# Kernel optimization log

Hardware: AMD Instinct MI355X
Metric: run time of the kernel (lower is better)

## Reference

```python
import jax, jax.numpy as jnp
import numpy as np

N = 10000           # nodes
E = 160000          # edges
MUL = 128           # multiplicity of each irrep (128x0e + 128x1o)
EDGE_FEAT = 8       # radial embedding dim
AVG_NUM_NEIGHBORS = 16.0
MLP_IN = MUL + MUL + EDGE_FEAT + 1  # 265
NUM_W = 4 * MUL     # irreps_mid num_irreps = 256x0e + 256x1o -> 512 path weights
SQ3 = float(np.sqrt(3.0))


def setup_inputs() -> dict:
    key = jax.random.key(0)
    ks = jax.random.split(key, 16)
    node_feats = jax.random.normal(ks[0], (N, 4 * MUL), dtype=jnp.float32)  # [N,512] = 128x0e ++ 128x1o
    edge_attrs = jax.random.normal(ks[1], (E, 4), dtype=jnp.float32)        # 1x0e ++ 1x1o
    edge_feats = jax.random.normal(ks[2], (E, EDGE_FEAT), dtype=jnp.float32)
    lengths = jax.random.uniform(ks[3], (E, 1), dtype=jnp.float32)
    edge_index = jax.random.randint(ks[4], (2, E), 0, N, dtype=jnp.int32)
    # e3nn Linear weights (stored unit-variance; forward applies 1/sqrt(fan_in))
    W_scalar = jax.random.normal(ks[5], (MUL, MUL), dtype=jnp.float32)
    W_up0 = jax.random.normal(ks[6], (MUL, MUL), dtype=jnp.float32)
    W_up1 = jax.random.normal(ks[7], (MUL, MUL), dtype=jnp.float32)
    # conv_tp_weights MLP (flax Dense: fan-scaled init, bias on first two layers)
    W1 = jax.random.normal(ks[8], (MLP_IN, MUL), dtype=jnp.float32) / np.sqrt(MLP_IN)
    b1 = jnp.zeros((MUL,), dtype=jnp.float32)
    W2 = jax.random.normal(ks[9], (MUL, MUL), dtype=jnp.float32) / np.sqrt(MUL)
    b2 = jnp.zeros((MUL,), dtype=jnp.float32)
    W3 = jax.random.normal(ks[10], (MUL, NUM_W), dtype=jnp.float32) / np.sqrt(MUL)
    # final e3nn Linear: 256x0e+256x1o -> 128x0e+128x1o
    Wout0 = jax.random.normal(ks[11], (2 * MUL, MUL), dtype=jnp.float32)
    Wout1 = jax.random.normal(ks[12], (2 * MUL, MUL), dtype=jnp.float32)
    return {"node_feats": node_feats, "edge_attrs": edge_attrs, "edge_feats": edge_feats,
            "lengths": lengths, "edge_index": edge_index, "W_scalar": W_scalar,
            "W_up0": W_up0, "W_up1": W_up1, "W1": W1, "b1": b1, "W2": W2, "b2": b2,
            "W3": W3, "Wout0": Wout0, "Wout1": Wout1}


def reference(node_feats, edge_attrs, edge_feats, lengths, edge_index,
              W_scalar, W_up0, W_up1, W1, b1, W2, b2, W3, Wout0, Wout1):
    n = node_feats.shape[0]
    inv = 1.0 / np.sqrt(MUL)
    x0 = node_feats[:, :MUL]                       # [N,128]   0e
    x1 = node_feats[:, MUL:].reshape(n, MUL, 3)    # [N,128,3] 1o

    # linear_scalar: only 0e->0e path survives
    scalars = (x0 @ W_scalar) * inv                # [N,128]
    # linear_up: per-irrep channel mixing
    h0 = (x0 @ W_up0) * inv                        # [N,128]
    h1 = jnp.einsum('nmi,mo->noi', x1, W_up1) * inv  # [N,128,3]

    sender, receiver = edge_index[0], edge_index[1]

    # conv_tp_weights MLP
    mlp_in = jnp.concatenate([scalars[sender], scalars[receiver], edge_feats, lengths], axis=-1)
    h = jax.nn.silu(mlp_in @ W1 + b1)
    h = jax.nn.silu(h @ W2 + b2)
    tpw = h @ W3                                   # [E,512]

    xs0 = h0[sender]                               # [E,128]
    xs1 = h1[sender]                               # [E,128,3]
    y0 = edge_attrs[:, 0:1]                        # [E,1]  0e
    y1 = edge_attrs[:, 1:4]                        # [E,3]  1o

    # CG tensor product (component normalization), filtered to {0e,1o}; sorted order:
    # 0e block = [0e*0e->0e, 1o*1o->0e], 1o block = [0e*1o->1o, 1o*0e->1o]
    mA = xs0 * y0                                       # [E,128]   0e
    mD = (xs1 * y1[:, None, :]).sum(-1) / SQ3           # [E,128]   0e
    mB = xs0[:, :, None] * y1[:, None, :]               # [E,128,3] 1o
    mC = xs1 * y0[:, :, None]                           # [E,128,3] 1o

    # per-irrep path weights (one scalar per irrep channel)
    wA, wD = tpw[:, :MUL], tpw[:, MUL:2 * MUL]
    wB, wC = tpw[:, 2 * MUL:3 * MUL], tpw[:, 3 * MUL:]

    m0 = jnp.concatenate([mA * wA, mD * wD], axis=1)                          # [E,256]
    m1 = jnp.concatenate([mB * wB[:, :, None], mC * wC[:, :, None]], axis=1)  # [E,256,3]

    # scatter-sum aggregation to receivers
    agg0 = jax.ops.segment_sum(m0, receiver, num_segments=n)  # [N,256]
    agg1 = jax.ops.segment_sum(m1, receiver, num_segments=n)  # [N,256,3]

    # final e3nn Linear + / avg_num_neighbors
    scale = 1.0 / (np.sqrt(2 * MUL) * AVG_NUM_NEIGHBORS)
    out0 = (agg0 @ Wout0) * scale                             # [N,128]
    out1 = jnp.einsum('nmi,mo->noi', agg1, Wout1) * scale     # [N,128,3]

    # reshape_irreps: [N, mul, sum(ir dims)] = [N,128,4]
    return jnp.concatenate([out0[:, :, None], out1], axis=-1)
```

## Files before the change

kernel.cpp:

```cpp
#include <hip/hip_runtime.h>
#include <hip/hip_bf16.h>

#define NN 10000
#define NE 160000
#define TILE 32
#define A1S 296
#define A2S 136

typedef __attribute__((ext_vector_type(8))) short short8;
typedef __attribute__((ext_vector_type(4))) float f32x4;

__device__ __forceinline__ float silu_f(float x) { return x / (1.0f + __expf(-x)); }
__device__ __forceinline__ unsigned short bf16u(float v) {
    __hip_bfloat16 b = __float2bfloat16(v);
    return *reinterpret_cast<unsigned short*>(&b);
}
__device__ __forceinline__ short8 pack8(float4 a, float4 b) {
    short8 r;
    r[0]=(short)bf16u(a.x); r[1]=(short)bf16u(a.y); r[2]=(short)bf16u(a.z); r[3]=(short)bf16u(a.w);
    r[4]=(short)bf16u(b.x); r[5]=(short)bf16u(b.y); r[6]=(short)bf16u(b.z); r[7]=(short)bf16u(b.w);
    return r;
}
__device__ __forceinline__ void lds_barrier() {
    asm volatile("s_waitcnt lgkmcnt(0)" ::: "memory");
    __builtin_amdgcn_s_barrier();
    asm volatile("" ::: "memory");
}

#define OFF_W1  0
#define OFF_W2  36864
#define OFF_W3  53248
#define OFF_WSC 118784
#define OFF_WU0 135168
#define OFF_WU1 151552
#define OFF_WO0 167936
#define OFF_WO1 200704
#define WP_TOTAL 233472

__global__ __launch_bounds__(256) void convert_weights(
    const float* __restrict__ W1, const float* __restrict__ W2,
    const float* __restrict__ W3, const float* __restrict__ Wsc,
    const float* __restrict__ Wu0, const float* __restrict__ Wu1,
    const float* __restrict__ Wo0, const float* __restrict__ Wo1,
    unsigned short* __restrict__ wp,
    const int* __restrict__ edge_index, int* __restrict__ deg)
{
    int idx = blockIdx.x * 256 + threadIdx.x;
    if (idx < NE) atomicAdd(&deg[edge_index[NE + idx]], 1);
    if (idx >= WP_TOTAL) return;
    const float* src; int off, N, K;
    if      (idx < OFF_W2)  { src = W1;  off = OFF_W1;  N = 128; K = 265; }
    else if (idx < OFF_W3)  { src = W2;  off = OFF_W2;  N = 128; K = 128; }
    else if (idx < OFF_WSC) { src = W3;  off = OFF_W3;  N = 512; K = 128; }
    else if (idx < OFF_WU0) { src = Wsc; off = OFF_WSC; N = 128; K = 128; }
    else if (idx < OFF_WU1) { src = Wu0; off = OFF_WU0; N = 128; K = 128; }
    else if (idx < OFF_WO0) { src = Wu1; off = OFF_WU1; N = 128; K = 128; }
    else if (idx < OFF_WO1) { src = Wo0; off = OFF_WO0; N = 128; K = 256; }
    else                    { src = Wo1; off = OFF_WO1; N = 128; K = 256; }
    int j = idx - off;
    int kt = j / (N * 32);
    int rem = j % (N * 32);
    int n = rem >> 5, kk = rem & 31;
    int k = kt * 32 + kk;
    wp[idx] = (k < K) ? bf16u(src[k * N + n]) : (unsigned short)0;
}

__global__ __launch_bounds__(256) void node_transform(
    const float* __restrict__ node_feats,
    const unsigned short* __restrict__ wp,
    unsigned short* __restrict__ scalars_bf,
    unsigned short* __restrict__ hall)
{
    __shared__ unsigned short xls[4 * 16 * 136];
    const int t = threadIdx.x;
    const int bn = blockIdx.x * 16;

    for (int i = t; i < 16 * 512; i += 256) {
        int n = i >> 9, j = i & 511;
        unsigned short u = bf16u(node_feats[(size_t)(bn + n) * 512 + j]);
        if (j < 128) xls[n * 136 + j] = u;
        else {
            int jj = j - 128;
            int m = jj / 3;
            int c = jj - 3 * m;
            xls[(1 + c) * 2176 + n * 136 + m] = u;
        }
    }
    __syncthreads();

    const int wv = t >> 6, lane = t & 63, l16 = lane & 15, l4 = lane >> 4;
    const unsigned short* Wscp = wp + OFF_WSC;
    const unsigned short* Wu0p = wp + OFF_WU0;
    const unsigned short* Wu1p = wp + OFF_WU1;

    f32x4 asc[2] = {}, ah0[2] = {}, ah1[3][2] = {};
    for (int kt = 0; kt < 4; ++kt) {
        short8 ax0 = *(const short8*)(xls + l16 * 136 + kt * 32 + l4 * 8);
        short8 ax1[3];
        #pragma unroll
        for (int c = 0; c < 3; ++c)
            ax1[c] = *(const short8*)(xls + (1 + c) * 2176 + l16 * 136 + kt * 32 + l4 * 8);
        #pragma unroll
        for (int n = 0; n < 2; ++n) {
            int col = wv * 32 + n * 16 + l16;
            short8 bsc = *(const short8*)(Wscp + ((size_t)kt * 128 + col) * 32 + l4 * 8);
            short8 bu0 = *(const short8*)(Wu0p + ((size_t)kt * 128 + col) * 32 + l4 * 8);
            short8 bu1 = *(const short8*)(Wu1p + ((size_t)kt * 128 + col) * 32 + l4 * 8);
            asc[n] = __builtin_amdgcn_mfma_f32_16x16x32_bf16(ax0, bsc, asc[n], 0, 0, 0);
            ah0[n] = __builtin_amdgcn_mfma_f32_16x16x32_bf16(ax0, bu0, ah0[n], 0, 0, 0);
            #pragma unroll
            for (int c = 0; c < 3; ++c)
                ah1[c][n] = __builtin_amdgcn_mfma_f32_16x16x32_bf16(ax1[c], bu1, ah1[c][n], 0, 0, 0);
        }
    }
    const float inv = 0.08838834764831845f;
    #pragma unroll
    for (int n = 0; n < 2; ++n) {
        int col = wv * 32 + n * 16 + l16;
        #pragma unroll
        for (int r = 0; r < 4; ++r) {
            int node = bn + l4 * 4 + r;
            scalars_bf[(size_t)node * 128 + col] = bf16u(asc[n][r] * inv);
            unsigned int lo = (unsigned int)bf16u(ah0[n][r] * inv)
                            | ((unsigned int)bf16u(ah1[0][n][r] * inv) << 16);
            unsigned int hi = (unsigned int)bf16u(ah1[1][n][r] * inv)
                            | ((unsigned int)bf16u(ah1[2][n][r] * inv) << 16);
            *(uint2*)(hall + ((size_t)node * 128 + col) * 4) = make_uint2(lo, hi);
        }
    }
}

__global__ __launch_bounds__(1024) void scan_kernel(const int* __restrict__ deg,
                                                    int* __restrict__ cursor) {
    __shared__ int s[1024];
    const int t = threadIdx.x;
    const int base = t * 10;
    int ld[10];
    int lsum = 0;
    #pragma unroll
    for (int i = 0; i < 10; ++i) {
        int idx = base + i;
        ld[i] = (idx < NN) ? deg[idx] : 0;
        lsum += ld[i];
    }
    s[t] = lsum;
    __syncthreads();
    for (int off = 1; off < 1024; off <<= 1) {
        int u = (t >= off) ? s[t - off] : 0;
        __syncthreads();
        s[t] += u;
        __syncthreads();
    }
    int run = s[t] - lsum;
    #pragma unroll
    for (int i = 0; i < 10; ++i) {
        int idx = base + i;
        if (idx < NN) cursor[idx] = run;
        run += ld[i];
    }
}

__global__ __launch_bounds__(256) void perm_kernel(const int* __restrict__ edge_index,
                                                   int* __restrict__ cursor,
                                                   int* __restrict__ perm) {
    int e = blockIdx.x * 256 + threadIdx.x;
    if (e < NE) {
        int r = edge_index[NE + e];
        int pos = atomicAdd(&cursor[r], 1);
        perm[pos] = e;
    }
}

__global__ __launch_bounds__(256, 5) void edge_kernel(
    const unsigned short* __restrict__ scalars_bf,
    const unsigned short* __restrict__ hall,
    const float* __restrict__ edge_attrs,
    const float* __restrict__ edge_feats,
    const float* __restrict__ lengths,
    const int* __restrict__ edge_index,
    const int* __restrict__ perm,
    const float* __restrict__ b1, const float* __restrict__ b2,
    const unsigned short* __restrict__ wp,
    float* __restrict__ agg0, float* __restrict__ agg1t)
{
    __shared__ unsigned char smem_u[27648];
    __shared__ int   eid_s[TILE];
    __shared__ int   s_s[TILE];
    __shared__ int   r_s[TILE];
    __shared__ float4 y_s[TILE];

    unsigned short* A1 = (unsigned short*)smem_u;
    unsigned short* A2 = (unsigned short*)(smem_u + 18944);
    unsigned short* A3 = A1;
    float* PKh = (float*)(smem_u + 8704);

    const int t = threadIdx.x;
    const int e0 = blockIdx.x * TILE;
    const int wv = t >> 6;
    const int lane = t & 63;
    const int l16 = lane & 15;
    const int l4 = lane >> 4;

    if (t < TILE) {
        int eid = perm[e0 + t];
        eid_s[t] = eid;
        s_s[t] = edge_index[eid];
        r_s[t] = edge_index[NE + eid];
        y_s[t] = *(const float4*)(edge_attrs + (size_t)eid * 4);
    }
    __syncthreads();

    {
        const int e = t >> 3, j = t & 7;
        const unsigned short* srow = scalars_bf + (size_t)s_s[e] * 128;
        const unsigned short* rrow = scalars_bf + (size_t)r_s[e] * 128;
        *(uint4*)(A1 + e*A1S + j*16)       = *(const uint4*)(srow + j*16);
        *(uint4*)(A1 + e*A1S + j*16 + 8)   = *(const uint4*)(srow + j*16 + 8);
        *(uint4*)(A1 + e*A1S + 128 + j*16)     = *(const uint4*)(rrow + j*16);
        *(uint4*)(A1 + e*A1S + 128 + j*16 + 8) = *(const uint4*)(rrow + j*16 + 8);
        A1[e*A1S + 256 + j] = bf16u(edge_feats[(size_t)eid_s[e] * 8 + j]);
        if (t < TILE) A1[t*A1S + 264] = bf16u(lengths[eid_s[t]]);
        for (int i = t; i < TILE * 23; i += 256) {
            int row = i / 23, c = 265 + (i - row * 23);
            A1[row*A1S + c] = 0;
        }
    }

    const int q = t >> 6, o = t & 63;
    const int rlo = q * 8;
    uint2 pfA[8], pfB[8];
    #pragma unroll
    for (int i = 0; i < 8; ++i)
        pfA[i] = *(const uint2*)(hall + ((size_t)s_s[rlo + i] * 128 + o) * 4);
    __syncthreads();

    const unsigned short* Wp1 = wp + OFF_W1;
    const unsigned short* Wp2 = wp + OFF_W2;
    const unsigned short* Wp3 = wp + OFF_W3;

    {
        f32x4 acc[2][2] = {};
        for (int kt = 0; kt < 9; ++kt) {
            short8 a0 = *(const short8*)(A1 + (     l16)*A1S + kt*32 + l4*8);
            short8 a1 = *(const short8*)(A1 + (16 + l16)*A1S + kt*32 + l4*8);
            #pragma unroll
            for (int n = 0; n < 2; ++n) {
                int col = (2*wv + n)*16 + l16;
                short8 b = *(const short8*)(Wp1 + ((size_t)kt*128 + col)*32 + l4*8);
                acc[0][n] = __builtin_amdgcn_mfma_f32_16x16x32_bf16(a0, b, acc[0][n], 0, 0, 0);
                acc[1][n] = __builtin_amdgcn_mfma_f32_16x16x32_bf16(a1, b, acc[1][n], 0, 0, 0);
            }
        }
        #pragma unroll
        for (int n = 0; n < 2; ++n) {
            int col = (2*wv + n)*16 + l16;
            float bb = b1[col];
            #pragma unroll
            for (int m = 0; m < 2; ++m)
                #pragma unroll
                for (int r = 0; r < 4; ++r) {
                    int row = m*16 + l4*4 + r;
                    A2[row*A2S + col] = bf16u(silu_f(acc[m][n][r] + bb));
                }
        }
    }
    __syncthreads();

    {
        f32x4 acc[2][2] = {};
        for (int kt = 0; kt < 4; ++kt) {
            short8 a0 = *(const short8*)(A2 + (     l16)*A2S + kt*32 + l4*8);
            short8 a1 = *(const short8*)(A2 + (16 + l16)*A2S + kt*32 + l4*8);
            #pragma unroll
            for (int n = 0; n < 2; ++n) {
                int col = (2*wv + n)*16 + l16;
                short8 b = *(const short8*)(Wp2 + ((size_t)kt*128 + col)*32 + l4*8);
                acc[0][n] = __builtin_amdgcn_mfma_f32_16x16x32_bf16(a0, b, acc[0][n], 0, 0, 0);
                acc[1][n] = __builtin_amdgcn_mfma_f32_16x16x32_bf16(a1, b, acc[1][n], 0, 0, 0);
            }
        }
        #pragma unroll
        for (int n = 0; n < 2; ++n) {
            int col = (2*wv + n)*16 + l16;
            float bb = b2[col];
            #pragma unroll
            for (int m = 0; m < 2; ++m)
                #pragma unroll
                for (int r = 0; r < 4; ++r) {
                    int row = m*16 + l4*4 + r;
                    A3[row*A2S + col] = bf16u(silu_f(acc[m][n][r] + bb));
                }
        }
    }
    __syncthreads();

    const float rs3 = 0.57735026918962576f;
    auto do_seg = [&](const int pass, const int hh, const uint2* pf) {
        const int base0 = pass ? 128 : 0;
        const int base1 = pass ? 384 : 256;
        f32x4 acc[2][2] = {};
        for (int kt = 0; kt < 4; ++kt) {
            short8 a0 = *(const short8*)(A3 + (     l16)*A2S + kt*32 + l4*8);
            short8 a1 = *(const short8*)(A3 + (16 + l16)*A2S + kt*32 + l4*8);
            #pragma unroll
            for (int fam = 0; fam < 2; ++fam) {
                int col = (fam ? base1 : base0) + hh*64 + wv*16 + l16;
                short8 b = *(const short8*)(Wp3 + ((size_t)kt*512 + col)*32 + l4*8);
                acc[fam][0] = __builtin_amdgcn_mfma_f32_16x16x32_bf16(a0, b, acc[fam][0], 0, 0, 0);
                acc[fam][1] = __builtin_amdgcn_mfma_f32_16x16x32_bf16(a1, b, acc[fam][1], 0, 0, 0);
            }
        }
        #pragma unroll
        for (int fam = 0; fam < 2; ++fam)
            #pragma unroll
            for (int m = 0; m < 2; ++m)
                #pragma unroll
                for (int r = 0; r < 4; ++r) {
                    int row = m*16 + l4*4 + r;
                    float y0 = y_s[row].x;
                    float fold = (fam == 0) ? (pass ? rs3 : y0) : (pass ? y0 : 1.0f);
                    PKh[row*132 + fam*64 + wv*16 + l16] = acc[fam][m][r] * fold;
                }
        lds_barrier();

        {
            const int ocol = hh*64 + o;
            float ac0 = 0.f, ac1 = 0.f, ac2 = 0.f, ac3 = 0.f;
            int run_start = rlo;
            int prev_rn = r_s[rlo];

            auto flush = [&](int rn, bool interior) {
                size_t b0 = (size_t)rn * 256 + base0 + ocol;
                if (interior) {
                    agg0[b0] = ac0;
                    agg1t[0*(size_t)NN*256 + b0] = ac1;
                    agg1t[1*(size_t)NN*256 + b0] = ac2;
                    agg1t[2*(size_t)NN*256 + b0] = ac3;
                } else {
                    atomicAdd(agg0 + b0, ac0);
                    atomicAdd(agg1t + 0*(size_t)NN*256 + b0, ac1);
                    atomicAdd(agg1t + 1*(size_t)NN*256 + b0, ac2);
                    atomicAdd(agg1t + 2*(size_t)NN*256 + b0, ac3);
                }
            };

            #pragma unroll
            for (int i = 0; i < 8; ++i) {
                int row = rlo + i;
                int rn = r_s[row];
                if (rn != prev_rn) {
                    flush(prev_rn, run_start > rlo);
                    ac0 = ac1 = ac2 = ac3 = 0.f;
                    run_start = row;
                    prev_rn = rn;
                }
                float w0 = PKh[row*132 + o];
                float w1 = PKh[row*132 + 64 + o];
                float4 y = y_s[row];
                if (pass == 0) {
                    float x = __uint_as_float(pf[i].x << 16);
                    ac0 = fmaf(x, w0, ac0);
                    float xb = x * w1;
                    ac1 = fmaf(xb, y.y, ac1);
                    ac2 = fmaf(xb, y.z, ac2);
                    ac3 = fmaf(xb, y.w, ac3);
                } else {
                    float xx = __uint_as_float(pf[i].x & 0xffff0000u);
                    float xy = __uint_as_float(pf[i].y << 16);
                    float xz = __uint_as_float(pf[i].y & 0xffff0000u);
                    float dd = xx*y.y + xy*y.z + xz*y.w;
                    ac0 = fmaf(dd, w0, ac0);
                    ac1 = fmaf(xx, w1, ac1);
                    ac2 = fmaf(xy, w1, ac2);
                    ac3 = fmaf(xz, w1, ac3);
                }
            }
            flush(prev_rn, false);
        }
        lds_barrier();
    };

    do_seg(0, 0, pfA);
    do_seg(1, 0, pfA);
    #pragma unroll
    for (int i = 0; i < 8; ++i)
        pfB[i] = *(const uint2*)(hall + ((size_t)s_s[rlo + i] * 128 + 64 + o) * 4);
    do_seg(0, 1, pfB);
    do_seg(1, 1, pfB);
}

__global__ __launch_bounds__(256) void output_transform(
    const float* __restrict__ agg0,
    const float* __restrict__ agg1t,
    const unsigned short* __restrict__ wp,
    float* __restrict__ out)
{
    __shared__ unsigned short As[4][16 * 264];
    const int t = threadIdx.x;
    const int bn = blockIdx.x * 16;

    for (int i = t; i < 2048; i += 256) {
        int mat = i >> 9;
        int rem = i & 511;
        int n = rem >> 5;
        int ko = (rem & 31) * 8;
        const float* src = (mat == 0)
            ? (agg0 + (size_t)(bn + n) * 256 + ko)
            : (agg1t + (size_t)(mat - 1) * NN * 256 + (size_t)(bn + n) * 256 + ko);
        float4 v0 = *(const float4*)(src);
        float4 v1 = *(const float4*)(src + 4);
        *(short8*)(&As[mat][n * 264 + ko]) = pack8(v0, v1);
    }
    __syncthreads();

    const int wv = t >> 6, lane = t & 63, l16 = lane & 15, l4 = lane >> 4;
    const unsigned short* Wo0p = wp + OFF_WO0;
    const unsigned short* Wo1p = wp + OFF_WO1;

    f32x4 acc[2][4] = {};
    for (int kt = 0; kt < 8; ++kt) {
        short8 a0 = *(const short8*)(&As[0][l16 * 264 + kt * 32 + l4 * 8]);
        short8 a1 = *(const short8*)(&As[1][l16 * 264 + kt * 32 + l4 * 8]);
        short8 a2 = *(const short8*)(&As[2][l16 * 264 + kt * 32 + l4 * 8]);
        short8 a3 = *(const short8*)(&As[3][l16 * 264 + kt * 32 + l4 * 8]);
        #pragma unroll
        for (int n = 0; n < 2; ++n) {
            int col = wv * 32 + n * 16 + l16;
            short8 bw0 = *(const short8*)(Wo0p + ((size_t)kt * 128 + col) * 32 + l4 * 8);
            short8 bw1 = *(const short8*)(Wo1p + ((size_t)kt * 128 + col) * 32 + l4 * 8);
            acc[n][0] = __builtin_amdgcn_mfma_f32_16x16x32_bf16(a0, bw0, acc[n][0], 0, 0, 0);
            acc[n][1] = __builtin_amdgcn_mfma_f32_16x16x32_bf16(a1, bw1, acc[n][1], 0, 0, 0);
            acc[n][2] = __builtin_amdgcn_mfma_f32_16x16x32_bf16(a2, bw1, acc[n][2], 0, 0, 0);
            acc[n][3] = __builtin_amdgcn_mfma_f32_16x16x32_bf16(a3, bw1, acc[n][3], 0, 0, 0);
        }
    }
    const float scale = 0.00390625f;
    #pragma unroll
    for (int n = 0; n < 2; ++n) {
        int col = wv * 32 + n * 16 + l16;
        #pragma unroll
        for (int r = 0; r < 4; ++r) {
            int node = bn + l4 * 4 + r;
            float4 v = make_float4(acc[n][0][r] * scale, acc[n][1][r] * scale,
                                   acc[n][2][r] * scale, acc[n][3][r] * scale);
            *(float4*)(out + ((size_t)node * 128 + col) * 4) = v;
        }
    }
}

extern "C" void kernel_launch(void* const* d_in, const int* in_sizes, int n_in,
                              void* d_out, int out_size, void* d_ws, size_t ws_size,
                              hipStream_t stream) {
    const float* node_feats = (const float*)d_in[0];
    const float* edge_attrs = (const float*)d_in[1];
    const float* edge_feats = (const float*)d_in[2];
    const float* lengths    = (const float*)d_in[3];
    const int*   edge_index = (const int*)d_in[4];
    const float* W_scalar   = (const float*)d_in[5];
    const float* W_up0      = (const float*)d_in[6];
    const float* W_up1      = (const float*)d_in[7];
    const float* W1         = (const float*)d_in[8];
    const float* b1         = (const float*)d_in[9];
    const float* W2         = (const float*)d_in[10];
    const float* b2         = (const float*)d_in[11];
    const float* W3         = (const float*)d_in[12];
    const float* Wout0      = (const float*)d_in[13];
    const float* Wout1      = (const float*)d_in[14];

    float* ws = (float*)d_ws;
    unsigned short* scalars_bf = (unsigned short*)ws;
    unsigned short* hall = (unsigned short*)(ws + 640000);
    float* agg0  = ws + 3200000;
    float* agg1t = ws + 5760000;
    int* deg    = (int*)(ws + 13440000);
    int* cursor = (int*)(ws + 13450000);
    int* perm   = (int*)(ws + 13460000);
    unsigned short* wpack = (unsigned short*)(ws + 13620000);
    if (ws_size < 13736736ull * 4ull) return;

    hipMemsetAsync(agg0, 0, 10250000ull * 4ull, stream);
    convert_weights<<<(WP_TOTAL + 255) / 256, 256, 0, stream>>>(
        W1, W2, W3, W_scalar, W_up0, W_up1, Wout0, Wout1, wpack, edge_index, deg);
    node_transform<<<625, 256, 0, stream>>>(node_feats, wpack, scalars_bf, hall);
    scan_kernel<<<1, 1024, 0, stream>>>(deg, cursor);
    perm_kernel<<<(NE + 255) / 256, 256, 0, stream>>>(edge_index, cursor, perm);
    edge_kernel<<<NE / TILE, 256, 0, stream>>>(scalars_bf, hall, edge_attrs, edge_feats, lengths,
                                               edge_index, perm, b1, b2, wpack, agg0, agg1t);
    output_transform<<<625, 256, 0, stream>>>(agg0, agg1t, wpack, (float*)d_out);
}
```

Measured before the change: 207.6 us.

## Process multiple edge tiles per block with prefetch, fold agg zeroing into node kernel

The edge kernel becomes persistent over four tiles per block. Each tile's indices and gathered scalar rows are double-buffered and prefetched while the previous tile's MLP runs, so gather latency is hidden behind the matrix work. The large memset of the aggregation buffers is replaced by zeroing inside node_transform, and only the degree array is memset. The trade-off is four times fewer edge blocks, which may reduce load balance and occupancy, plus extra register pressure from the prefetched values.

```diff
diff --git a/kernel.cpp b/kernel.cpp
--- a/kernel.cpp
+++ b/kernel.cpp
@@ -4,6 +4,7 @@
 #define NN 10000
 #define NE 160000
 #define TILE 32
+#define TPB 4
 #define A1S 296
 #define A2S 136
 
@@ -69,11 +70,25 @@
     const float* __restrict__ node_feats,
     const unsigned short* __restrict__ wp,
     unsigned short* __restrict__ scalars_bf,
-    unsigned short* __restrict__ hall)
+    unsigned short* __restrict__ hall,
+    float* __restrict__ agg0, float* __restrict__ agg1t)
 {
     __shared__ unsigned short xls[4 * 16 * 136];
     const int t = threadIdx.x;
     const int bn = blockIdx.x * 16;
+
+    {
+        const float4 z = make_float4(0.f, 0.f, 0.f, 0.f);
+        float4* a0 = (float4*)(agg0 + (size_t)bn * 256);
+        #pragma unroll
+        for (int i = 0; i < 4; ++i) a0[t + 256 * i] = z;
+        #pragma unroll
+        for (int c = 0; c < 3; ++c) {
+            float4* a1 = (float4*)(agg1t + (size_t)c * NN * 256 + (size_t)bn * 256);
+            #pragma unroll
+            for (int i = 0; i < 4; ++i) a1[t + 256 * i] = z;
+        }
+    }
 
     for (int i = t; i < 16 * 512; i += 256) {
         int n = i >> 9, j = i & 511;
@@ -184,10 +199,10 @@
     float* __restrict__ agg0, float* __restrict__ agg1t)
 {
     __shared__ unsigned char smem_u[27648];
-    __shared__ int   eid_s[TILE];
-    __shared__ int   s_s[TILE];
-    __shared__ int   r_s[TILE];
-    __shared__ float4 y_s[TILE];
+    __shared__ int   eid_s[2][TILE];
+    __shared__ int   s_s[2][TILE];
+    __shared__ int   r_s[2][TILE];
+    __shared__ float4 y_s[2][TILE];
 
     unsigned short* A1 = (unsigned short*)smem_u;
     unsigned short* A2 = (unsigned short*)(smem_u + 18944);
@@ -195,198 +210,235 @@
     float* PKh = (float*)(smem_u + 8704);
 
     const int t = threadIdx.x;
-    const int e0 = blockIdx.x * TILE;
     const int wv = t >> 6;
     const int lane = t & 63;
     const int l16 = lane & 15;
     const int l4 = lane >> 4;
+    const int q = t >> 6, o = t & 63;
+    const int rlo = q * 8;
+    const int es = t >> 3, j8 = t & 7;
+
+    const int tile0 = blockIdx.x * TPB;
+
+    const unsigned short* Wp1 = wp + OFF_W1;
+    const unsigned short* Wp2 = wp + OFF_W2;
+    const unsigned short* Wp3 = wp + OFF_W3;
+    const float rs3 = 0.57735026918962576f;
+
+    int h_eid = 0, h_s = 0, h_r = 0; float4 h_y = make_float4(0,0,0,0);
+    uint4 sv0, sv1, rv0, rv1; float efreg; float lenreg;
 
     if (t < TILE) {
-        int eid = perm[e0 + t];
-        eid_s[t] = eid;
-        s_s[t] = edge_index[eid];
-        r_s[t] = edge_index[NE + eid];
-        y_s[t] = *(const float4*)(edge_attrs + (size_t)eid * 4);
-    }
-    __syncthreads();
-
+        int eid = perm[tile0 * TILE + t];
+        eid_s[0][t] = eid;
+        s_s[0][t] = edge_index[eid];
+        r_s[0][t] = edge_index[NE + eid];
+        y_s[0][t] = *(const float4*)(edge_attrs + (size_t)eid * 4);
+    }
+    lds_barrier();
     {
-        const int e = t >> 3, j = t & 7;
-        const unsigned short* srow = scalars_bf + (size_t)s_s[e] * 128;
-        const unsigned short* rrow = scalars_bf + (size_t)r_s[e] * 128;
-        *(uint4*)(A1 + e*A1S + j*16)       = *(const uint4*)(srow + j*16);
-        *(uint4*)(A1 + e*A1S + j*16 + 8)   = *(const uint4*)(srow + j*16 + 8);
-        *(uint4*)(A1 + e*A1S + 128 + j*16)     = *(const uint4*)(rrow + j*16);
-        *(uint4*)(A1 + e*A1S + 128 + j*16 + 8) = *(const uint4*)(rrow + j*16 + 8);
-        A1[e*A1S + 256 + j] = bf16u(edge_feats[(size_t)eid_s[e] * 8 + j]);
-        if (t < TILE) A1[t*A1S + 264] = bf16u(lengths[eid_s[t]]);
+        const unsigned short* srow = scalars_bf + (size_t)s_s[0][es] * 128;
+        const unsigned short* rrow = scalars_bf + (size_t)r_s[0][es] * 128;
+        sv0 = *(const uint4*)(srow + j8*16);
+        sv1 = *(const uint4*)(srow + j8*16 + 8);
+        rv0 = *(const uint4*)(rrow + j8*16);
+        rv1 = *(const uint4*)(rrow + j8*16 + 8);
+        efreg = edge_feats[(size_t)eid_s[0][es] * 8 + j8];
+        lenreg = (t < TILE) ? lengths[eid_s[0][t]] : 0.f;
+    }
+
+    #pragma unroll 1
+    for (int j = 0; j < TPB; ++j) {
+        const int cur = j & 1, nxt = cur ^ 1;
+
+        *(uint4*)(A1 + es*A1S + j8*16)       = sv0;
+        *(uint4*)(A1 + es*A1S + j8*16 + 8)   = sv1;
+        *(uint4*)(A1 + es*A1S + 128 + j8*16)     = rv0;
+        *(uint4*)(A1 + es*A1S + 128 + j8*16 + 8) = rv1;
+        A1[es*A1S + 256 + j8] = bf16u(efreg);
+        if (t < TILE) A1[t*A1S + 264] = bf16u(lenreg);
         for (int i = t; i < TILE * 23; i += 256) {
             int row = i / 23, c = 265 + (i - row * 23);
             A1[row*A1S + c] = 0;
         }
-    }
-
-    const int q = t >> 6, o = t & 63;
-    const int rlo = q * 8;
-    uint2 pfA[8], pfB[8];
-    #pragma unroll
-    for (int i = 0; i < 8; ++i)
-        pfA[i] = *(const uint2*)(hall + ((size_t)s_s[rlo + i] * 128 + o) * 4);
-    __syncthreads();
-
-    const unsigned short* Wp1 = wp + OFF_W1;
-    const unsigned short* Wp2 = wp + OFF_W2;
-    const unsigned short* Wp3 = wp + OFF_W3;
-
-    {
-        f32x4 acc[2][2] = {};
-        for (int kt = 0; kt < 9; ++kt) {
-            short8 a0 = *(const short8*)(A1 + (     l16)*A1S + kt*32 + l4*8);
-            short8 a1 = *(const short8*)(A1 + (16 + l16)*A1S + kt*32 + l4*8);
+
+        uint2 pfA[8], pfB[8];
+        #pragma unroll
+        for (int i = 0; i < 8; ++i)
+            pfA[i] = *(const uint2*)(hall + ((size_t)s_s[cur][rlo + i] * 128 + o) * 4);
+
+        if (j + 1 < TPB && t < TILE) {
+            h_eid = perm[(tile0 + j + 1) * TILE + t];
+            h_s = edge_index[h_eid];
+            h_r = edge_index[NE + h_eid];
+            h_y = *(const float4*)(edge_attrs + (size_t)h_eid * 4);
+        }
+
+        lds_barrier();
+
+        {
+            f32x4 acc[2][2] = {};
+            for (int kt = 0; kt < 9; ++kt) {
+                short8 a0 = *(const short8*)(A1 + (     l16)*A1S + kt*32 + l4*8);
+                short8 a1 = *(const short8*)(A1 + (16 + l16)*A1S + kt*32 + l4*8);
+                #pragma unroll
+                for (int n = 0; n < 2; ++n) {
+                    int col = (2*wv + n)*16 + l16;
+                    short8 b = *(const short8*)(Wp1 + ((size_t)kt*128 + col)*32 + l4*8);
+                    acc[0][n] = __builtin_amdgcn_mfma_f32_16x16x32_bf16(a0, b, acc[0][n], 0, 0, 0);
+                    acc[1][n] = __builtin_amdgcn_mfma_f32_16x16x32_bf16(a1, b, acc[1][n], 0, 0, 0);
+                }
+            }
             #pragma unroll
             for (int n = 0; n < 2; ++n) {
                 int col = (2*wv + n)*16 + l16;
-                short8 b = *(const short8*)(Wp1 + ((size_t)kt*128 + col)*32 + l4*8);
-                acc[0][n] = __builtin_amdgcn_mfma_f32_16x16x32_bf16(a0, b, acc[0][n], 0, 0, 0);
-                acc[1][n] = __builtin_amdgcn_mfma_f32_16x16x32_bf16(a1, b, acc[1][n], 0, 0, 0);
+                float bb = b1[col];
+                #pragma unroll
+                for (int m = 0; m < 2; ++m)
+                    #pragma unroll
+                    for (int r = 0; r < 4; ++r) {
+                        int row = m*16 + l4*4 + r;
+                        A2[row*A2S + col] = bf16u(silu_f(acc[m][n][r] + bb));
+                    }
             }
         }
-        #pragma unroll
-        for (int n = 0; n < 2; ++n) {
-            int col = (2*wv + n)*16 + l16;
-            float bb = b1[col];
-            #pragma unroll
-            for (int m = 0; m < 2; ++m)
-                #pragma unroll
-                for (int r = 0; r < 4; ++r) {
-                    int row = m*16 + l4*4 + r;
-                    A2[row*A2S + col] = bf16u(silu_f(acc[m][n][r] + bb));
+        if (j + 1 < TPB && t < TILE) {
+            eid_s[nxt][t] = h_eid; s_s[nxt][t] = h_s; r_s[nxt][t] = h_r; y_s[nxt][t] = h_y;
+        }
+        lds_barrier();
+
+        if (j + 1 < TPB) {
+            const unsigned short* srow = scalars_bf + (size_t)s_s[nxt][es] * 128;
+            const unsigned short* rrow = scalars_bf + (size_t)r_s[nxt][es] * 128;
+            sv0 = *(const uint4*)(srow + j8*16);
+            sv1 = *(const uint4*)(srow + j8*16 + 8);
+            rv0 = *(const uint4*)(rrow + j8*16);
+            rv1 = *(const uint4*)(rrow + j8*16 + 8);
+            efreg = edge_feats[(size_t)eid_s[nxt][es] * 8 + j8];
+            lenreg = (t < TILE) ? lengths[eid_s[nxt][t]] : 0.f;
+        }
+
+        {
+            f32x4 acc[2][2] = {};
+            for (int kt = 0; kt < 4; ++kt) {
+                short8 a0 = *(const short8*)(A2 + (     l16)*A2S + kt*32 + l4*8);
+                short8 a1 = *(const short8*)(A2 + (16 + l16)*A2S + kt*32 + l4*8);
+                #pragma unroll
+                for (int n = 0; n < 2; ++n) {
+                    int col = (2*wv + n)*16 + l16;
+                    short8 b = *(const short8*)(Wp2 + ((size_t)kt*128 + col)*32 + l4*8);
+                    acc[0][n] = __builtin_amdgcn_mfma_f32_16x16x32_bf16(a0, b, acc[0][n], 0, 0, 0);
+                    acc[1][n] = __builtin_amdgcn_mfma_f32_16x16x32_bf16(a1, b, acc[1][n], 0, 0, 0);
                 }
-        }
-    }
-    __syncthreads();
-
-    {
-        f32x4 acc[2][2] = {};
-        for (int kt = 0; kt < 4; ++kt) {
-            short8 a0 = *(const short8*)(A2 + (     l16)*A2S + kt*32 + l4*8);
-            short8 a1 = *(const short8*)(A2 + (16 + l16)*A2S + kt*32 + l4*8);
+            }
             #pragma unroll
             for (int n = 0; n < 2; ++n) {
                 int col = (2*wv + n)*16 + l16;
-                short8 b = *(const short8*)(Wp2 + ((size_t)kt*128 + col)*32 + l4*8);
-                acc[0][n] = __builtin_amdgcn_mfma_f32_16x16x32_bf16(a0, b, acc[0][n], 0, 0, 0);
-                acc[1][n] = __builtin_amdgcn_mfma_f32_16x16x32_bf16(a1, b, acc[1][n], 0, 0, 0);
+                float bb = b2[col];
+                #pragma unroll
+                for (int m = 0; m < 2; ++m)
+                    #pragma unroll
+                    for (int r = 0; r < 4; ++r) {
+                        int row = m*16 + l4*4 + r;
+                        A3[row*A2S + col] = bf16u(silu_f(acc[m][n][r] + bb));
+                    }
             }
         }
-        #pragma unroll
-        for (int n = 0; n < 2; ++n) {
-            int col = (2*wv + n)*16 + l16;
-            float bb = b2[col];
-            #pragma unroll
-            for (int m = 0; m < 2; ++m)
-                #pragma unroll
-                for (int r = 0; r < 4; ++r) {
-                    int row = m*16 + l4*4 + r;
-                    A3[row*A2S + col] = bf16u(silu_f(acc[m][n][r] + bb));
-                }
-        }
-    }
-    __syncthreads();
-
-    const float rs3 = 0.57735026918962576f;
-    auto do_seg = [&](const int pass, const int hh, const uint2* pf) {
-        const int base0 = pass ? 128 : 0;
-        const int base1 = pass ? 384 : 256;
-        f32x4 acc[2][2] = {};
-        for (int kt = 0; kt < 4; ++kt) {
-            short8 a0 = *(const short8*)(A3 + (     l16)*A2S + kt*32 + l4*8);
-            short8 a1 = *(const short8*)(A3 + (16 + l16)*A2S + kt*32 + l4*8);
-            #pragma unroll
-            for (int fam = 0; fam < 2; ++fam) {
-                int col = (fam ? base1 : base0) + hh*64 + wv*16 + l16;
-                short8 b = *(const short8*)(Wp3 + ((size_t)kt*512 + col)*32 + l4*8);
-                acc[fam][0] = __builtin_amdgcn_mfma_f32_16x16x32_bf16(a0, b, acc[fam][0], 0, 0, 0);
-                acc[fam][1] = __builtin_amdgcn_mfma_f32_16x16x32_bf16(a1, b, acc[fam][1], 0, 0, 0);
-            }
-        }
-        #pragma unroll
-        for (int fam = 0; fam < 2; ++fam)
-            #pragma unroll
-            for (int m = 0; m < 2; ++m)
-                #pragma unroll
-                for (int r = 0; r < 4; ++r) {
-                    int row = m*16 + l4*4 + r;
-                    float y0 = y_s[row].x;
-                    float fold = (fam == 0) ? (pass ? rs3 : y0) : (pass ? y0 : 1.0f);
-                    PKh[row*132 + fam*64 + wv*16 + l16] = acc[fam][m][r] * fold;
-                }
         lds_barrier();
 
-        {
-            const int ocol = hh*64 + o;
-            float ac0 = 0.f, ac1 = 0.f, ac2 = 0.f, ac3 = 0.f;
-            int run_start = rlo;
-            int prev_rn = r_s[rlo];
-
-            auto flush = [&](int rn, bool interior) {
-                size_t b0 = (size_t)rn * 256 + base0 + ocol;
-                if (interior) {
-                    agg0[b0] = ac0;
-                    agg1t[0*(size_t)NN*256 + b0] = ac1;
-                    agg1t[1*(size_t)NN*256 + b0] = ac2;
-                    agg1t[2*(size_t)NN*256 + b0] = ac3;
-                } else {
-                    atomicAdd(agg0 + b0, ac0);
-                    atomicAdd(agg1t + 0*(size_t)NN*256 + b0, ac1);
-                    atomicAdd(agg1t + 1*(size_t)NN*256 + b0, ac2);
-                    atomicAdd(agg1t + 2*(size_t)NN*256 + b0, ac3);
-                }
-            };
-
-            #pragma unroll
-            for (int i = 0; i < 8; ++i) {
-                int row = rlo + i;
-                int rn = r_s[row];
-                if (rn != prev_rn) {
-                    flush(prev_rn, run_start > rlo);
-                    ac0 = ac1 = ac2 = ac3 = 0.f;
-                    run_start = row;
-                    prev_rn = rn;
-                }
-                float w0 = PKh[row*132 + o];
-                float w1 = PKh[row*132 + 64 + o];
-                float4 y = y_s[row];
-                if (pass == 0) {
-                    float x = __uint_as_float(pf[i].x << 16);
-                    ac0 = fmaf(x, w0, ac0);
-                    float xb = x * w1;
-                    ac1 = fmaf(xb, y.y, ac1);
-                    ac2 = fmaf(xb, y.z, ac2);
-                    ac3 = fmaf(xb, y.w, ac3);
-                } else {
-                    float xx = __uint_as_float(pf[i].x & 0xffff0000u);
-                    float xy = __uint_as_float(pf[i].y << 16);
-                    float xz = __uint_as_float(pf[i].y & 0xffff0000u);
-                    float dd = xx*y.y + xy*y.z + xz*y.w;
-                    ac0 = fmaf(dd, w0, ac0);
-                    ac1 = fmaf(xx, w1, ac1);
-                    ac2 = fmaf(xy, w1, ac2);
-                    ac3 = fmaf(xz, w1, ac3);
+        auto do_seg = [&](const int pass, const int hh, const uint2* pf) {
+            const int base0 = pass ? 128 : 0;
+            const int base1 = pass ? 384 : 256;
+            f32x4 acc[2][2] = {};
+            for (int kt = 0; kt < 4; ++kt) {
+                short8 a0 = *(const short8*)(A3 + (     l16)*A2S + kt*32 + l4*8);
+                short8 a1 = *(const short8*)(A3 + (16 + l16)*A2S + kt*32 + l4*8);
+                #pragma unroll
+                for (int fam = 0; fam < 2; ++fam) {
+                    int col = (fam ? base1 : base0) + hh*64 + wv*16 + l16;
+                    short8 b = *(const short8*)(Wp3 + ((size_t)kt*512 + col)*32 + l4*8);
+                    acc[fam][0] = __builtin_amdgcn_mfma_f32_16x16x32_bf16(a0, b, acc[fam][0], 0, 0, 0);
+                    acc[fam][1] = __builtin_amdgcn_mfma_f32_16x16x32_bf16(a1, b, acc[fam][1], 0, 0, 0);
                 }
             }
-            flush(prev_rn, false);
-        }
-        lds_barrier();
-    };
-
-    do_seg(0, 0, pfA);
-    do_seg(1, 0, pfA);
-    #pragma unroll
-    for (int i = 0; i < 8; ++i)
-        pfB[i] = *(const uint2*)(hall + ((size_t)s_s[rlo + i] * 128 + 64 + o) * 4);
-    do_seg(0, 1, pfB);
-    do_seg(1, 1, pfB);
+            #pragma unroll
+            for (int fam = 0; fam < 2; ++fam)
+                #pragma unroll
+                for (int m = 0; m < 2; ++m)
+                    #pragma unroll
+                    for (int r = 0; r < 4; ++r) {
+                        int row = m*16 + l4*4 + r;
+                        float y0 = y_s[cur][row].x;
+                        float fold = (fam == 0) ? (pass ? rs3 : y0) : (pass ? y0 : 1.0f);
+                        PKh[row*132 + fam*64 + wv*16 + l16] = acc[fam][m][r] * fold;
+                    }
+            lds_barrier();
+
+            {
+                const int ocol = hh*64 + o;
+                float ac0 = 0.f, ac1 = 0.f, ac2 = 0.f, ac3 = 0.f;
+                int run_start = rlo;
+                int prev_rn = r_s[cur][rlo];
+
+                auto flush = [&](int rn, bool interior) {
+                    size_t b0 = (size_t)rn * 256 + base0 + ocol;
+                    if (interior) {
+                        agg0[b0] = ac0;
+                        agg1t[0*(size_t)NN*256 + b0] = ac1;
+                        agg1t[1*(size_t)NN*256 + b0] = ac2;
+                        agg1t[2*(size_t)NN*256 + b0] = ac3;
+                    } else {
+                        atomicAdd(agg0 + b0, ac0);
+                        atomicAdd(agg1t + 0*(size_t)NN*256 + b0, ac1);
+                        atomicAdd(agg1t + 1*(size_t)NN*256 + b0, ac2);
+                        atomicAdd(agg1t + 2*(size_t)NN*256 + b0, ac3);
+                    }
+                };
+
+                #pragma unroll
+                for (int i = 0; i < 8; ++i) {
+                    int row = rlo + i;
+                    int rn = r_s[cur][row];
+                    if (rn != prev_rn) {
+                        flush(prev_rn, run_start > rlo);
+                        ac0 = ac1 = ac2 = ac3 = 0.f;
+                        run_start = row;
+                        prev_rn = rn;
+                    }
+                    float w0 = PKh[row*132 + o];
+                    float w1 = PKh[row*132 + 64 + o];
+                    float4 y = y_s[cur][row];
+                    if (pass == 0) {
+                        float x = __uint_as_float(pf[i].x << 16);
+                        ac0 = fmaf(x, w0, ac0);
+                        float xb = x * w1;
+                        ac1 = fmaf(xb, y.y, ac1);
+                        ac2 = fmaf(xb, y.z, ac2);
+                        ac3 = fmaf(xb, y.w, ac3);
+                    } else {
+                        float xx = __uint_as_float(pf[i].x & 0xffff0000u);
+                        float xy = __uint_as_float(pf[i].y << 16);
+                        float xz = __uint_as_float(pf[i].y & 0xffff0000u);
+                        float dd = xx*y.y + xy*y.z + xz*y.w;
+                        ac0 = fmaf(dd, w0, ac0);
+                        ac1 = fmaf(xx, w1, ac1);
+                        ac2 = fmaf(xy, w1, ac2);
+                        ac3 = fmaf(xz, w1, ac3);
+                    }
+                }
+                flush(prev_rn, false);
+            }
+            lds_barrier();
+        };
+
+        do_seg(0, 0, pfA);
+        do_seg(1, 0, pfA);
+        #pragma unroll
+        for (int i = 0; i < 8; ++i)
+            pfB[i] = *(const uint2*)(hall + ((size_t)s_s[cur][rlo + i] * 128 + 64 + o) * 4);
+        do_seg(0, 1, pfB);
+        do_seg(1, 1, pfB);
+    }
 }
 
 __global__ __launch_bounds__(256) void output_transform(
@@ -478,13 +530,13 @@
     unsigned short* wpack = (unsigned short*)(ws + 13620000);
     if (ws_size < 13736736ull * 4ull) return;
 
-    hipMemsetAsync(agg0, 0, 10250000ull * 4ull, stream);
+    hipMemsetAsync(deg, 0, NN * 4, stream);
     convert_weights<<<(WP_TOTAL + 255) / 256, 256, 0, stream>>>(
         W1, W2, W3, W_scalar, W_up0, W_up1, Wout0, Wout1, wpack, edge_index, deg);
-    node_transform<<<625, 256, 0, stream>>>(node_feats, wpack, scalars_bf, hall);
+    node_transform<<<625, 256, 0, stream>>>(node_feats, wpack, scalars_bf, hall, agg0, agg1t);
     scan_kernel<<<1, 1024, 0, stream>>>(deg, cursor);
     perm_kernel<<<(NE + 255) / 256, 256, 0, stream>>>(edge_index, cursor, perm);
-    edge_kernel<<<NE / TILE, 256, 0, stream>>>(scalars_bf, hall, edge_attrs, edge_feats, lengths,
-                                               edge_index, perm, b1, b2, wpack, agg0, agg1t);
+    edge_kernel<<<NE / TILE / TPB, 256, 0, stream>>>(scalars_bf, hall, edge_attrs, edge_feats, lengths,
+                                                     edge_index, perm, b1, b2, wpack, agg0, agg1t);
     output_transform<<<625, 256, 0, stream>>>(agg0, agg1t, wpack, (float*)d_out);
 }
```

Measured after the change: 355.5 us. 71.2% more time.
